# Performance work log

Measured on AMD Instinct MI355X. Metric: run time of the kernel, lower is better.

The kernel has to match this reference:

```python
import jax, jax.numpy as jnp
import numpy as np

NX = NY = NZ = 128
B = 4
WEIGHT_RESIDU = 1.0
EPS_NEEDLE = 1e-6  # self.epsilon_needle


def lap1d(u, axis):
    """1D Neumann Laplacian (ordre=1) along `axis`: interior [1,-2,1], boundary rows [-1,1]/[1,-1]."""
    u = jnp.moveaxis(u, axis, 0)
    lap = -2.0 * u
    lap = lap.at[:-1].add(u[1:]).at[1:].add(u[:-1])
    # boundary fix: row0 = -u0 + u1, rowN-1 = u_{N-2} - u_{N-1}
    lap = lap.at[0].add(u[0]).at[-1].add(u[-1])
    return jnp.moveaxis(lap, 0, axis)


def setup_inputs() -> dict:
    key = jax.random.key(0)
    k1, k2, k3 = jax.random.split(key, 3)
    output = jax.random.normal(k1, (B, 1, NX, NY, NZ), dtype=jnp.float32)
    gt = jax.random.normal(k2, (B, 1, NX, NY, NZ), dtype=jnp.float32)
    # trinary field in {-1, 0, 1}: g = (input==1), f = (input==-1) + g
    inp = (jax.random.randint(k3, (B, 1, NX, NY, NZ), 0, 3) - 1).astype(jnp.float32)
    return {"output": output, "gt": gt, "input": inp}


def reference(output, gt, input):
    nx, ny, nz = gt.shape[-3], gt.shape[-2], gt.shape[-1]
    dx = 2.0 / (nx - 1)
    dy = 2.0 / (ny - 1)
    dz = 2.0 / (nz - 1)
    a1 = dy / dx
    a2 = dz / dx
    dx2 = dx * dx

    # diagonal of A = -Lap3DNeu (ordre=1): 2 interior / 1 at ends per axis
    def dvec(n):
        return jnp.full((n,), 2.0, dtype=jnp.float32).at[0].set(1.0).at[-1].set(1.0)

    diag_lap = (dvec(nx)[:, None, None]
                + dvec(ny)[None, :, None] / a1**2
                + dvec(nz)[None, None, :] / a2**2)  # (nx,ny,nz)

    # boundary zeroing of b decodes flat index as k*nx*ny + j*nx + i -> (nz,ny,nx) view
    interior = (jnp.zeros((nz, ny, nx), dtype=jnp.float32)
                .at[1:-1, 1:-1, 1:-1].set(1.0).reshape(-1))

    def per_sample(u, img):
        g = (img == 1.0).astype(u.dtype)
        f = (img == -1.0).astype(u.dtype) + g
        f_div_eps = f * (dx2 / EPS_NEEDLE)  # conductivity == 1
        # A_full @ u : 7-point Neumann stencil + needle diagonal
        Au = -(lap1d(u, 0) + lap1d(u, 1) / a1**2 + lap1d(u, 2) / a2**2) + f_div_eps * u
        b = (g * f_div_eps).reshape(-1) * interior
        mx = jnp.max(diag_lap + f_div_eps)  # == torch.max(A_full.to_dense())
        res = jnp.abs(Au.reshape(-1) - b) / mx * (1.0 - f.reshape(-1))
        return WEIGHT_RESIDU * res

    res = jax.vmap(per_sample)(output[:, 0], input[:, 0])  # (B, nx*ny*nz)
    return jnp.mean(res)
```

## Files before the change

### kernel.cpp

```cpp
#include <hip/hip_runtime.h>


namespace {
constexpr int NDIM  = 128;
constexpr int PL    = NDIM * NDIM;
constexpr int NPS   = NDIM * NDIM * NDIM;
constexpr int BATCH = 4;
constexpr int BLOCKS_PER_S = 1024;
constexpr int NBLOCKS = BATCH * BLOCKS_PER_S;
}

__device__ __forceinline__ void stencil4(
        const float4& c, const float4& xm, const float4& xp,
        const float4& ym, const float4& yp, float lf_raw, float rg_raw,
        const float4& g, bool klo, bool khi, float dij, const float* dkt,
        float C, float& sum, float& mx) {
    float cc[4] = {c.x, c.y, c.z, c.w};
    float zl[4] = {klo ? c.x : lf_raw, c.x, c.y, c.z};
    float zr[4] = {c.y, c.z, c.w, khi ? c.w : rg_raw};
    float im[4] = {xm.x, xm.y, xm.z, xm.w};
    float ip[4] = {xp.x, xp.y, xp.z, xp.w};
    float jm[4] = {ym.x, ym.y, ym.z, ym.w};
    float jp[4] = {yp.x, yp.y, yp.z, yp.w};
    float gg[4] = {g.x, g.y, g.z, g.w};
#pragma unroll
    for (int t = 0; t < 4; ++t) {
        float lap = (im[t] + ip[t]) + (jm[t] + jp[t]) + (zl[t] + zr[t]) - 6.0f * cc[t];
        bool needle = (gg[t] != 0.0f);
        sum += needle ? 0.0f : fabsf(lap);
        mx = fmaxf(mx, dij + dkt[t] + (needle ? C : 0.0f));
    }
}

__global__ __launch_bounds__(256, 8) void loss_main_k(
        const float* __restrict__ u, const float* __restrict__ img,
        float* __restrict__ psum, float* __restrict__ pmax, float C) {
    int blk = blockIdx.x;
    int b   = blk >> 10;
    int q   = blk & (BLOCKS_PER_S - 1);
    int t   = threadIdx.x;
    int i   = q >> 3;
    int j0  = (q & 7) * 8 + ((t >> 5) & 7);
    int kv  = t & 31;
    int k4  = kv << 2;

    const float* ub = u   + (size_t)b * NPS;
    const float* gb = img + (size_t)b * NPS;
    int rowA = (i * NDIM + 2 * j0) * NDIM + k4;

    int ojm = (j0 == 0)  ? 0 : -NDIM;
    int ojp = (j0 == 63) ? 0 :  NDIM;
    int oim = (i == 0)          ? 0 : -PL;
    int oip = (i == NDIM - 1)   ? 0 :  PL;
    float di  = (i == 0 || i == NDIM - 1) ? 1.0f : 2.0f;
    float djA = (j0 == 0)  ? 1.0f : 2.0f;
    float djB = (j0 == 63) ? 1.0f : 2.0f;
    float dkt[4] = { (kv == 0) ? 1.0f : 2.0f, 2.0f, 2.0f,
                     (kv == 31) ? 1.0f : 2.0f };
    bool klo = (kv == 0), khi = (kv == 31);

    const float* pa = ub + rowA;
    float4 cA  = *(const float4*)pa;
    float4 cB  = *(const float4*)(pa + NDIM);
    float4 ymA = *(const float4*)(pa + ojm);
    float4 ypB = *(const float4*)(pa + NDIM + ojp);
    float4 xmA = *(const float4*)(pa + oim);
    float4 xmB = *(const float4*)(pa + oim + NDIM);
    float4 xpA = *(const float4*)(pa + oip);
    float4 xpB = *(const float4*)(pa + oip + NDIM);
    const float* pg = gb + rowA;
    float4 gA  = *(const float4*)pg;
    float4 gB  = *(const float4*)(pg + NDIM);

    float sum = 0.0f, mx = 0.0f;
    float lfA = __shfl_up(cA.w, 1), rgA = __shfl_down(cA.x, 1);
    float lfB = __shfl_up(cB.w, 1), rgB = __shfl_down(cB.x, 1);
    stencil4(cA, xmA, xpA, ymA, cB, lfA, rgA, gA, klo, khi, di + djA, dkt, C, sum, mx);
    stencil4(cB, xmB, xpB, cA, ypB, lfB, rgB, gB, klo, khi, di + djB, dkt, C, sum, mx);

#pragma unroll
    for (int off = 32; off > 0; off >>= 1) {
        sum += __shfl_down(sum, off);
        mx = fmaxf(mx, __shfl_down(mx, off));
    }
    __shared__ float ssum[4], smax[4];
    int wave = threadIdx.x >> 6, lane = threadIdx.x & 63;
    if (lane == 0) { ssum[wave] = sum; smax[wave] = mx; }
    __syncthreads();
    if (threadIdx.x == 0) {
        psum[blk] = (ssum[0] + ssum[1]) + (ssum[2] + ssum[3]);
        pmax[blk] = fmaxf(fmaxf(smax[0], smax[1]), fmaxf(smax[2], smax[3]));
    }
}

__global__ __launch_bounds__(256) void finalize_k(const float* __restrict__ psum,
                                                  const float* __restrict__ pmax,
                                                  float* __restrict__ out) {
    int wave = threadIdx.x >> 6, lane = threadIdx.x & 63;
    double s = 0.0; float m = 0.0f;
    int base = wave * BLOCKS_PER_S;
#pragma unroll
    for (int r = 0; r < BLOCKS_PER_S / 64; ++r) {
        int idx = base + r * 64 + lane;
        s += (double)psum[idx];
        m = fmaxf(m, pmax[idx]);
    }
#pragma unroll
    for (int off = 32; off > 0; off >>= 1) {
        s += __shfl_down(s, off);
        m = fmaxf(m, __shfl_down(m, off));
    }
    __shared__ double ws[4]; __shared__ float wm[4];
    if (lane == 0) { ws[wave] = s; wm[wave] = m; }
    __syncthreads();
    if (threadIdx.x == 0) {
        double tot = 0.0;
        for (int b = 0; b < BATCH; ++b) tot += ws[b] / (double)wm[b];
        out[0] = (float)(tot / ((double)BATCH * (double)NPS));
    }
}

extern "C" void kernel_launch(void* const* d_in, const int* in_sizes, int n_in,
                              void* d_out, int out_size, void* d_ws, size_t ws_size,
                              hipStream_t stream) {
    const float* u   = (const float*)d_in[0];
    const float* img = (const float*)d_in[2];
    float* out = (float*)d_out;

    float* psum = (float*)d_ws;
    float* pmax = psum + NBLOCKS;

    const double dx = 2.0 / (NDIM - 1);
    const float  C  = (float)((dx * dx) / 1e-6);

    hipLaunchKernelGGL(loss_main_k, dim3(NBLOCKS), dim3(256), 0, stream,
                       u, img, psum, pmax, C);
    hipLaunchKernelGGL(finalize_k, dim3(1), dim3(256), 0, stream, psum, pmax, out);
}
```

Baseline: 18.41 us.

## Process two adjacent i-planes per thread to reuse neighbor loads; halve block count

After: 18.25 us. Within noise of the previous version (-0.9%).

```diff
diff --git a/kernel.cpp b/kernel.cpp
--- a/kernel.cpp
+++ b/kernel.cpp
@@ -6,7 +6,7 @@
 constexpr int PL    = NDIM * NDIM;
 constexpr int NPS   = NDIM * NDIM * NDIM;
 constexpr int BATCH = 4;
-constexpr int BLOCKS_PER_S = 1024;
+constexpr int BLOCKS_PER_S = 512;
 constexpr int NBLOCKS = BATCH * BLOCKS_PER_S;
 }
 
@@ -36,60 +36,88 @@
         const float* __restrict__ u, const float* __restrict__ img,
         float* __restrict__ psum, float* __restrict__ pmax, float C) {
     int blk = blockIdx.x;
-    int b   = blk >> 10;
+    int b   = blk >> 9;
     int q   = blk & (BLOCKS_PER_S - 1);
     int t   = threadIdx.x;
-    int i   = q >> 3;
+    int i0  = q >> 3;
     int j0  = (q & 7) * 8 + ((t >> 5) & 7);
     int kv  = t & 31;
     int k4  = kv << 2;
+    int iA  = 2 * i0;
+    int iB  = iA + 1;
 
     const float* ub = u   + (size_t)b * NPS;
     const float* gb = img + (size_t)b * NPS;
-    int rowA = (i * NDIM + 2 * j0) * NDIM + k4;
+    int base0 = (iA * NDIM + 2 * j0) * NDIM + k4;
+    int base1 = base0 + PL;
 
     int ojm = (j0 == 0)  ? 0 : -NDIM;
     int ojp = (j0 == 63) ? 0 :  NDIM;
-    int oim = (i == 0)          ? 0 : -PL;
-    int oip = (i == NDIM - 1)   ? 0 :  PL;
-    float di  = (i == 0 || i == NDIM - 1) ? 1.0f : 2.0f;
+    int oim = (iA == 0)        ? 0 : -PL;
+    int oip = (iB == NDIM - 1) ? 0 :  PL;
+    float di0 = (iA == 0)        ? 1.0f : 2.0f;
+    float di1 = (iB == NDIM - 1) ? 1.0f : 2.0f;
     float djA = (j0 == 0)  ? 1.0f : 2.0f;
     float djB = (j0 == 63) ? 1.0f : 2.0f;
     float dkt[4] = { (kv == 0) ? 1.0f : 2.0f, 2.0f, 2.0f,
                      (kv == 31) ? 1.0f : 2.0f };
     bool klo = (kv == 0), khi = (kv == 31);
 
-    const float* pa = ub + rowA;
-    float4 cA  = *(const float4*)pa;
-    float4 cB  = *(const float4*)(pa + NDIM);
-    float4 ymA = *(const float4*)(pa + ojm);
-    float4 ypB = *(const float4*)(pa + NDIM + ojp);
-    float4 xmA = *(const float4*)(pa + oim);
-    float4 xmB = *(const float4*)(pa + oim + NDIM);
-    float4 xpA = *(const float4*)(pa + oip);
-    float4 xpB = *(const float4*)(pa + oip + NDIM);
-    const float* pg = gb + rowA;
-    float4 gA  = *(const float4*)pg;
-    float4 gB  = *(const float4*)(pg + NDIM);
+    float sum = 0.0f, mx = 0.0f;
 
-    float sum = 0.0f, mx = 0.0f;
-    float lfA = __shfl_up(cA.w, 1), rgA = __shfl_down(cA.x, 1);
-    float lfB = __shfl_up(cB.w, 1), rgB = __shfl_down(cB.x, 1);
-    stencil4(cA, xmA, xpA, ymA, cB, lfA, rgA, gA, klo, khi, di + djA, dkt, C, sum, mx);
-    stencil4(cB, xmB, xpB, cA, ypB, lfB, rgB, gB, klo, khi, di + djB, dkt, C, sum, mx);
+    const float* p0 = ub + base0;
+    const float* p1 = ub + base1;
+    float4 c0A = *(const float4*)p0;
+    float4 c0B = *(const float4*)(p0 + NDIM);
+    float4 c1A = *(const float4*)p1;
+    float4 c1B = *(const float4*)(p1 + NDIM);
+    float4 xmA = *(const float4*)(p0 + oim);
+    float4 xmB = *(const float4*)(p0 + oim + NDIM);
+    float4 ym0 = *(const float4*)(p0 + ojm);
+    float4 yp0 = *(const float4*)(p0 + NDIM + ojp);
+    const float* g0 = gb + base0;
+    float4 g0A = *(const float4*)g0;
+    float4 g0B = *(const float4*)(g0 + NDIM);
 
+    {
+        float lfA = __shfl_up(c0A.w, 1), rgA = __shfl_down(c0A.x, 1);
+        float lfB = __shfl_up(c0B.w, 1), rgB = __shfl_down(c0B.x, 1);
+        stencil4(c0A, xmA, c1A, ym0, c0B, lfA, rgA, g0A, klo, khi,
+                 di0 + djA, dkt, C, sum, mx);
+        stencil4(c0B, xmB, c1B, c0A, yp0, lfB, rgB, g0B, klo, khi,
+                 di0 + djB, dkt, C, sum, mx);
+    }
+
+    float4 xpA = *(const float4*)(p1 + oip);
+    float4 xpB = *(const float4*)(p1 + oip + NDIM);
+    float4 ym1 = *(const float4*)(p1 + ojm);
+    float4 yp1 = *(const float4*)(p1 + NDIM + ojp);
+    const float* g1 = gb + base1;
+    float4 g1A = *(const float4*)g1;
+    float4 g1B = *(const float4*)(g1 + NDIM);
+
+    {
+        float lfA = __shfl_up(c1A.w, 1), rgA = __shfl_down(c1A.x, 1);
+        float lfB = __shfl_up(c1B.w, 1), rgB = __shfl_down(c1B.x, 1);
+        stencil4(c1A, c0A, xpA, ym1, c1B, lfA, rgA, g1A, klo, khi,
+                 di1 + djA, dkt, C, sum, mx);
+        stencil4(c1B, c0B, xpB, c1A, yp1, lfB, rgB, g1B, klo, khi,
+                 di1 + djB, dkt, C, sum, mx);
+    }
+
+    __shared__ float2 red[256];
+    red[t] = make_float2(sum, mx);
+    __syncthreads();
+    if (t < 64) {
+        float2 a = red[t], b2 = red[t + 64], c2 = red[t + 128], d2 = red[t + 192];
+        float s = (a.x + b2.x) + (c2.x + d2.x);
+        float m = fmaxf(fmaxf(a.y, b2.y), fmaxf(c2.y, d2.y));
 #pragma unroll
-    for (int off = 32; off > 0; off >>= 1) {
-        sum += __shfl_down(sum, off);
-        mx = fmaxf(mx, __shfl_down(mx, off));
-    }
-    __shared__ float ssum[4], smax[4];
-    int wave = threadIdx.x >> 6, lane = threadIdx.x & 63;
-    if (lane == 0) { ssum[wave] = sum; smax[wave] = mx; }
-    __syncthreads();
-    if (threadIdx.x == 0) {
-        psum[blk] = (ssum[0] + ssum[1]) + (ssum[2] + ssum[3]);
-        pmax[blk] = fmaxf(fmaxf(smax[0], smax[1]), fmaxf(smax[2], smax[3]));
+        for (int off = 32; off > 0; off >>= 1) {
+            s += __shfl_down(s, off);
+            m = fmaxf(m, __shfl_down(m, off));
+        }
+        if (t == 0) { psum[blk] = s; pmax[blk] = m; }
     }
 }
 
```
